# Performance work log

Measured on AMD Instinct MI355X. Metric: run time of the kernel, lower is better.

The kernel has to match this reference:

```python
import jax, jax.numpy as jnp
import numpy as np

B, S, D = 4, 1024, 1024
NH, DH = 16, 64
DI = 4096
EPS = 1e-5


def layer_norm(x, g, b):
    mu = jnp.mean(x, axis=-1, keepdims=True)
    var = jnp.mean(jnp.square(x - mu), axis=-1, keepdims=True)
    return (x - mu) * jax.lax.rsqrt(var + EPS) * g + b


def rel_shift(x):
    # x: [B, n, q, r] -> Transformer-XL relative shift + lower-tri mask
    b, n, q, r = x.shape
    zp = jnp.zeros((b, n, q, 1), x.dtype)
    xp = jnp.concatenate([zp, x], axis=3).reshape(b, n, r + 1, q)
    x = xp[:, :, 1:, :].reshape(b, n, q, r)
    tril = jnp.tril(jnp.ones((q, r), x.dtype), r - q)
    return x * tril[None, None]


def setup_inputs() -> dict:
    key = jax.random.key(0)
    ks = jax.random.split(key, 16)
    sc = 0.02
    return {
        "w": jax.random.normal(ks[0], (B, S, D), jnp.float32),
        "r": jax.random.normal(ks[1], (B, S, D), jnp.float32),
        "w_bias": jax.random.normal(ks[2], (NH, 1, DH), jnp.float32) * sc,
        "r_bias": jax.random.normal(ks[3], (NH, 1, DH), jnp.float32) * sc,
        "Wq": jax.random.normal(ks[4], (D, NH * DH), jnp.float32) * sc,
        "Wk": jax.random.normal(ks[5], (D, NH * DH), jnp.float32) * sc,
        "Wv": jax.random.normal(ks[6], (D, NH * DH), jnp.float32) * sc,
        "Wr": jax.random.normal(ks[7], (D, NH * DH), jnp.float32) * sc,
        "Wo": jax.random.normal(ks[8], (NH * DH, D), jnp.float32) * sc,
        "ln1_g": jnp.ones((D,), jnp.float32),
        "ln1_b": jnp.zeros((D,), jnp.float32),
        "W1": jax.random.normal(ks[9], (D, DI), jnp.float32) * sc,
        "b1": jnp.zeros((DI,), jnp.float32),
        "W2": jax.random.normal(ks[10], (DI, D), jnp.float32) * sc,
        "b2": jnp.zeros((D,), jnp.float32),
        "ln2_g": jnp.ones((D,), jnp.float32),
        "ln2_b": jnp.zeros((D,), jnp.float32),
    }


def reference(w, r, w_bias, r_bias, Wq, Wk, Wv, Wr, Wo,
              ln1_g, ln1_b, W1, b1, W2, b2, ln2_g, ln2_b):
    b, q_len, _ = w.shape
    k_len = q_len
    scale = 1.0 / (DH ** 0.5)

    def heads(x):
        return x.reshape(b, -1, NH, DH).transpose(0, 2, 1, 3)  # [B, n, S, d]

    q = heads(w @ Wq)
    k = heads(w @ Wk)
    v = heads(w @ Wv)
    rr = heads(r @ Wr)

    ac = jnp.einsum('bnid,bnjd->bnij', q + w_bias[None], k)
    bd = rel_shift(jnp.einsum('bnid,bnjd->bnij', q + r_bias[None], rr))
    attn_score = (ac + bd) * scale

    mask = jnp.triu(jnp.ones((q_len, k_len), bool), 1)
    attn_score = jnp.where(mask[None, None], jnp.float32(-1e9), attn_score)
    attn_prob = jax.nn.softmax(attn_score, axis=-1)

    attn_vec = jnp.einsum('bnij,bnjd->bnid', attn_prob, v)
    attn_vec = attn_vec.transpose(0, 2, 1, 3).reshape(b, q_len, NH * DH)
    attn_out = attn_vec @ Wo

    x = layer_norm(w + attn_out, ln1_g, ln1_b)
    ff = jax.nn.relu(x @ W1 + b1) @ W2 + b2
    return layer_norm(x + ff, ln2_g, ln2_b)
```

## Files before the change

### kernel.cpp

```cpp
#include <hip/hip_runtime.h>
#include <hip/hip_bf16.h>

using bf16 = __hip_bfloat16;
typedef __attribute__((ext_vector_type(8))) short bf16x8;
typedef __attribute__((ext_vector_type(4))) float f32x4;

static constexpr int TB  = 4;
static constexpr int TS  = 1024;
static constexpr int TD  = 1024;
static constexpr int TNH = 16;
static constexpr int TDH = 64;
static constexpr int TDI = 4096;

__device__ __forceinline__ void gll16(const bf16* g, bf16* l)
{
    __builtin_amdgcn_global_load_lds(
        (const __attribute__((address_space(1))) void*)g,
        (__attribute__((address_space(3))) void*)l, 16, 0, 0);
}

__global__ __launch_bounds__(256) void zero_out_k(float* __restrict__ out, long n)
{
    long i = (long)blockIdx.x * 256 + threadIdx.x;
    if (i < n) out[i] = 0.0f;
}

__global__ __launch_bounds__(256) void convert2_f2b(const float* __restrict__ a,
                                                    const float* __restrict__ b,
                                                    bf16* __restrict__ oa,
                                                    bf16* __restrict__ ob, long n)
{
    const float* src = blockIdx.y ? b : a;
    bf16* dst = blockIdx.y ? ob : oa;
    long i = ((long)blockIdx.x * 256 + threadIdx.x) * 8;
    if (i >= n) return;
    float4 f0 = *(const float4*)(src + i);
    float4 f1 = *(const float4*)(src + i + 4);
    bf16 t[8] = {__float2bfloat16(f0.x), __float2bfloat16(f0.y),
                 __float2bfloat16(f0.z), __float2bfloat16(f0.w),
                 __float2bfloat16(f1.x), __float2bfloat16(f1.y),
                 __float2bfloat16(f1.z), __float2bfloat16(f1.w)};
    *(bf16x8*)(dst + i) = *(bf16x8*)t;
}

__global__ __launch_bounds__(256) void transpose_f2b(const float* __restrict__ in,
                                                     bf16* __restrict__ out,
                                                     int R, int C)
{
    __shared__ float tile[32][33];
    int c0 = blockIdx.x * 32, r0 = blockIdx.y * 32;
    int tx = threadIdx.x & 31, ty = threadIdx.x >> 5;
#pragma unroll
    for (int dy = 0; dy < 32; dy += 8)
        tile[ty + dy][tx] = in[(long)(r0 + ty + dy) * C + (c0 + tx)];
    __syncthreads();
#pragma unroll
    for (int dy = 0; dy < 32; dy += 8)
        out[(long)(c0 + ty + dy) * R + (r0 + tx)] = __float2bfloat16(tile[tx][ty + dy]);
}

__global__ __launch_bounds__(256) void transpose5_f2b(const float* __restrict__ p0,
                                                      const float* __restrict__ p1,
                                                      const float* __restrict__ p2,
                                                      const float* __restrict__ p3,
                                                      const float* __restrict__ p4,
                                                      bf16* __restrict__ dstBase)
{
    __shared__ float tile[32][33];
    const int D = TD;
    int z = blockIdx.z;
    const float* in = (z == 0) ? p0 : (z == 1) ? p1 : (z == 2) ? p2 : (z == 3) ? p3 : p4;
    bf16* out = dstBase + (long)z * D * D;
    int c0 = blockIdx.x * 32, r0 = blockIdx.y * 32;
    int tx = threadIdx.x & 31, ty = threadIdx.x >> 5;
#pragma unroll
    for (int dy = 0; dy < 32; dy += 8)
        tile[ty + dy][tx] = in[(long)(r0 + ty + dy) * D + (c0 + tx)];
    __syncthreads();
#pragma unroll
    for (int dy = 0; dy < 32; dy += 8)
        out[(long)(c0 + ty + dy) * D + (r0 + tx)] = __float2bfloat16(tile[tx][ty + dy]);
}

__global__ __launch_bounds__(256) void transpose_v(const bf16* __restrict__ V,
                                                   bf16* __restrict__ VT)
{
    __shared__ bf16 tile[32][33];
    int bn = blockIdx.z;
    int b = bn >> 4, n = bn & 15;
    const bf16* src = V + ((long)b * TS) * (TNH * TDH) + n * TDH;
    bf16* dst = VT + (long)bn * TDH * TS;
    int s0 = blockIdx.x * 32, d0 = blockIdx.y * 32;
    int tx = threadIdx.x & 31, ty = threadIdx.x >> 5;
#pragma unroll
    for (int dy = 0; dy < 32; dy += 8)
        tile[ty + dy][tx] = src[(long)(s0 + ty + dy) * (TNH * TDH) + (d0 + tx)];
    __syncthreads();
#pragma unroll
    for (int dy = 0; dy < 32; dy += 8)
        dst[(long)(d0 + ty + dy) * TS + (s0 + tx)] = tile[tx][ty + dy];
}


__device__ __forceinline__ void stage_half(const bf16* __restrict__ X, long ldx,
                                           long rbase, long kcol,
                                           bf16* lds, int srow)
{
    gll16(X + (rbase + srow) * ldx + kcol, lds);
    gll16(X + (rbase + 128 + srow) * ldx + kcol, lds + 4096);
}

template<int MODE>
__global__ __launch_bounds__(512, 2) void gemm256_k(
    const bf16* __restrict__ A, long lda,
    const bf16* __restrict__ Bt, long ldb,
    bf16* __restrict__ O0, bf16* __restrict__ O1,
    bf16* __restrict__ O2, bf16* __restrict__ O3,
    float* __restrict__ F0, float* __restrict__ F1,
    float* __restrict__ F2, float* __restrict__ F3,
    const float* __restrict__ bias,
    int Kz, int GY, long ldc)
{
    __shared__ bf16 LDSbf[65536];

    const int z = blockIdx.y;
    const long kb = (long)z * Kz;
    const int NT = Kz >> 6;
    const int NI = NT >> 1;

    const int nwg = gridDim.x;
    const int orig = blockIdx.x;
    const int q = nwg >> 3, r = nwg & 7;
    const int xcd = orig & 7, idx = orig >> 3;
    const int wgid = (xcd < r ? xcd * (q + 1) : r * (q + 1) + (xcd - r) * q) + idx;

    int tx, ty;
    if (MODE == 1) {
        if (wgid < 192) { ty = wgid & 15; tx = wgid >> 4; }
        else { int w2 = wgid - 192; ty = 16 + (w2 & 15); tx = 12 + (w2 >> 4); }
    } else {
        ty = wgid % GY; tx = wgid / GY;
    }
    const long row0 = (long)ty * 256;
    const int col0 = tx * 256;

    const int tid = threadIdx.x;
    const int lane = tid & 63;
    const int wave = tid >> 6;
    const int wm2 = wave >> 2;
    const int wn4 = wave & 3;
    const int l15 = lane & 15;
    const int lq  = lane >> 4;

    const int slot = ((l15 & 1) << 2) | (lq ^ ((l15 >> 1) & 3));
    const int rdA = (wm2 * 64 + (l15 >> 1)) * 64 + slot * 8;
    const int rdB = 16384 + (wn4 * 32 + (l15 >> 1)) * 64 + slot * 8;

    const int srow  = wave * 16 + ((lane >> 3) << 1) + ((lane >> 2) & 1);
    const int scol8 = ((lane & 3) ^ ((lane >> 3) & 3)) * 8;

    f32x4 acc[8][4] = {};
    bf16x8 af[8], bb[4];

#define SA(t, db, kh) stage_half(A, lda, row0, kb + (long)(t) * 64 + (kh) * 32 + scol8, \
                                 LDSbf + (db) * 32768 + (kh) * 8192 + wave * 512, srow)
#define SB(t, db, kh) stage_half(Bt, ldb, (long)col0, kb + (long)(t) * 64 + (kh) * 32 + scol8, \
                                 LDSbf + (db) * 32768 + 16384 + (kh) * 8192 + wave * 512, srow)
#define RD_A(bp, kh) do {                                                              \
    _Pragma("unroll")                                                                  \
    for (int i_ = 0; i_ < 8; ++i_)                                                     \
        af[i_] = *(const bf16x8*)(LDSbf + (bp) * 32768 + (kh) * 8192 + rdA + i_ * 512);\
    } while (0)
#define RD_B(bp, kh, jh) do {                                                          \
    bb[(jh)*2]   = *(const bf16x8*)(LDSbf + (bp)*32768 + (kh)*8192 + rdB + ((jh)*2)*512);   \
    bb[(jh)*2+1] = *(const bf16x8*)(LDSbf + (bp)*32768 + (kh)*8192 + rdB + ((jh)*2+1)*512); \
    } while (0)
#define MM(jh) do {                                                                    \
    __builtin_amdgcn_s_setprio(1);                                                     \
    _Pragma("unroll")                                                                  \
    for (int i_ = 0; i_ < 8; ++i_) {                                                   \
        acc[i_][(jh)*2]   = __builtin_amdgcn_mfma_f32_16x16x32_bf16(af[i_], bb[(jh)*2],   acc[i_][(jh)*2],   0, 0, 0); \
        acc[i_][(jh)*2+1] = __builtin_amdgcn_mfma_f32_16x16x32_bf16(af[i_], bb[(jh)*2+1], acc[i_][(jh)*2+1], 0, 0, 0); \
    }                                                                                  \
    __builtin_amdgcn_s_setprio(0);                                                     \
    } while (0)
#define BAR       __builtin_amdgcn_s_barrier()
#define WLGKM0    do { asm volatile("s_waitcnt lgkmcnt(0)" ::: "memory");              \
                       __builtin_amdgcn_sched_barrier(0); } while (0)
#define WVM6      asm volatile("s_waitcnt vmcnt(6)" ::: "memory")

    SA(0, 0, 0); SB(0, 0, 0); SA(0, 0, 1); SB(0, 0, 1); SA(1, 1, 0);
    WVM6; BAR;

    for (int it = 0; it < NI; ++it) {
        const int T  = 2 * it;
        const int t1 = T + 1;
        const int t2 = (T + 2 < NT) ? T + 2 : NT - 1;
        const int t3 = (T + 3 < NT) ? T + 3 : NT - 1;

        RD_A(0, 0); RD_B(0, 0, 0); SB(t1, 1, 0);
        BAR; WLGKM0; MM(0); BAR;
        RD_B(0, 0, 1); SA(t1, 1, 1);
        BAR; WLGKM0; MM(1); WVM6; BAR;
        RD_A(0, 1); RD_B(0, 1, 0); SB(t1, 1, 1);
        BAR; WLGKM0; MM(0); BAR;
        RD_B(0, 1, 1); SA(t2, 0, 0);
        BAR; WLGKM0; MM(1); WVM6; BAR;
        RD_A(1, 0); RD_B(1, 0, 0); SB(t2, 0, 0);
        BAR; WLGKM0; MM(0); BAR;
        RD_B(1, 0, 1); SA(t2, 0, 1);
        BAR; WLGKM0; MM(1); WVM6; BAR;
        RD_A(1, 1); RD_B(1, 1, 0); SB(t2, 0, 1);
        BAR; WLGKM0; MM(0); BAR;
        RD_B(1, 1, 1); SA(t3, 1, 0);
        BAR; WLGKM0; MM(1); WVM6; BAR;
    }
    asm volatile("s_waitcnt vmcnt(0)" ::: "memory");

#undef SA
#undef SB
#undef RD_A
#undef RD_B
#undef MM
#undef BAR
#undef WLGKM0
#undef WVM6

    if (MODE == 0) {
        float* F = (z == 0) ? F0 : (z == 1) ? F1 : (z == 2) ? F2 : F3;
#pragma unroll
        for (int i = 0; i < 8; ++i) {
            long rb = (row0 + wm2 * 128 + i * 16 + lq * 4) * ldc;
#pragma unroll
            for (int j = 0; j < 4; ++j) {
                int nc = col0 + wn4 * 64 + j * 16 + l15;
#pragma unroll
                for (int rg = 0; rg < 4; ++rg)
                    F[rb + (long)rg * ldc + nc] = acc[i][j][rg];
            }
        }
    } else if (MODE == 1) {
        const int sel = tx >> 2;
        bf16* O = (sel == 0) ? O0 : (sel == 1) ? O1 : (sel == 2) ? O2 : O3;
        const int coladj = sel << 10;
        const long rowadj = (sel == 3) ? 4096 : 0;
#pragma unroll
        for (int i = 0; i < 8; ++i) {
            long rb = (row0 - rowadj + wm2 * 128 + i * 16 + lq * 4) * 1024;
#pragma unroll
            for (int j = 0; j < 4; ++j) {
                int nc = col0 - coladj + wn4 * 64 + j * 16 + l15;
#pragma unroll
                for (int rg = 0; rg < 4; ++rg) {
                    float v = acc[i][j][rg];
                    if (sel == 0) v += bias[nc];
                    O[rb + (long)rg * 1024 + nc] = __float2bfloat16(v);
                }
            }
        }
    } else {
#pragma unroll
        for (int i = 0; i < 8; ++i) {
            long rb = (row0 + wm2 * 128 + i * 16 + lq * 4) * ldc;
#pragma unroll
            for (int j = 0; j < 4; ++j) {
                int nc = col0 + wn4 * 64 + j * 16 + l15;
#pragma unroll
                for (int rg = 0; rg < 4; ++rg) {
                    float v = acc[i][j][rg] + bias[nc];
                    v = fmaxf(v, 0.0f);
                    O0[rb + (long)rg * ldc + nc] = __float2bfloat16(v);
                }
            }
        }
    }
}

__global__ __launch_bounds__(256, 1) void flash_attn(
    const bf16* __restrict__ Qw, const bf16* __restrict__ Kb,
    const bf16* __restrict__ RRb, const bf16* __restrict__ VT,
    const float* __restrict__ wbias, const float* __restrict__ rbias,
    bf16* __restrict__ Oa)
{
    const int S = TS, D = TD;
    __shared__ bf16 Ks[128 * 64];
    __shared__ bf16 RRs[256 * 64];
    __shared__ bf16 VTs[64 * 128];
    __shared__ bf16 SCR[4][32 * 161];

    const int bx = blockIdx.x;
    const int irev = bx >> 6, bn = bx & 63;
    const int it = 7 - irev;
    const int i0 = it * 128;
    const int b = bn >> 4, n = bn & 15;

    const int tid = threadIdx.x, lane = tid & 63, wave = tid >> 6;
    const int dw = wave * 32;
    const int l15 = lane & 15, lq = lane >> 4;
    const int sr8 = lane >> 3, sc8 = lane & 7;
    const int vr4 = lane >> 4, vc16 = lane & 15;

    bf16x8 afw[2][2], afr[2][2];
#pragma unroll
    for (int m = 0; m < 2; ++m)
#pragma unroll
        for (int ks = 0; ks < 2; ++ks) {
            const bf16* qp = Qw + ((long)(b * S + i0 + dw + 16 * m + l15)) * D
                             + n * 64 + ks * 32 + lq * 8;
            afw[m][ks] = *(const bf16x8*)qp;
            bf16 tmp[8];
#pragma unroll
            for (int jj = 0; jj < 8; ++jj) {
                int di_ = n * 64 + ks * 32 + lq * 8 + jj;
                float f = __bfloat162float(((const bf16*)&afw[m][ks])[jj])
                          + rbias[di_] - wbias[di_];
                tmp[jj] = __float2bfloat16(f);
            }
            afr[m][ks] = *(bf16x8*)tmp;
        }

    float mst[2][4], lst[2][4];
    f32x4 Oacc[2][4] = {};
#pragma unroll
    for (int m = 0; m < 2; ++m)
#pragma unroll
        for (int rg = 0; rg < 4; ++rg) { mst[m][rg] = -1e30f; lst[m][rg] = 0.0f; }

    bf16* scr = &SCR[wave][0];
    const int cofs = 96 - dw;

    for (int jt = 0; jt <= it; ++jt) {
        const int j0 = jt * 128;
        const int cT0 = S - 1 + j0 - i0 - 127;

#pragma unroll
        for (int c = 0; c < 4; ++c) {
            int ch = wave * 4 + c;
            int row = ch * 8 + sr8;
            int cbs = sc8 ^ (sr8 & 7);
            gll16(Kb + ((long)(b * S + j0 + row)) * D + n * 64 + cbs * 8, &Ks[ch * 512]);
        }
#pragma unroll
        for (int c = 0; c < 8; ++c) {
            int ch = wave * 8 + c;
            int row = ch * 8 + sr8;
            int grow = cT0 + row; if (grow > S - 1) grow = S - 1;
            int cbs = sc8 ^ (sr8 & 7);
            gll16(RRb + ((long)(b * S + grow)) * D + n * 64 + cbs * 8, &RRs[ch * 512]);
        }
#pragma unroll
        for (int c = 0; c < 4; ++c) {
            int ch = wave * 4 + c;
            int row = ch * 4 + vr4;
            int cbs = vc16 ^ (row & 15);
            gll16(VT + ((long)(bn * 64 + row)) * S + j0 + cbs * 8, &VTs[ch * 512]);
        }
        __syncthreads();

        f32x4 bd[2][10] = {};
#pragma unroll
        for (int ks = 0; ks < 2; ++ks) {
            bf16x8 bfr[10];
#pragma unroll
            for (int nf = 0; nf < 10; ++nf) {
                int row = cofs + nf * 16 + l15;
                int cb = ks * 4 + lq;
                bfr[nf] = *(const bf16x8*)(&RRs[row * 64 + (cb ^ (row & 7)) * 8]);
            }
#pragma unroll
            for (int m = 0; m < 2; ++m)
#pragma unroll
                for (int nf = 0; nf < 10; ++nf)
                    bd[m][nf] = __builtin_amdgcn_mfma_f32_16x16x32_bf16(
                        afr[m][ks], bfr[nf], bd[m][nf], 0, 0, 0);
        }
#pragma unroll
        for (int m = 0; m < 2; ++m)
#pragma unroll
            for (int nf = 0; nf < 10; ++nf)
#pragma unroll
                for (int rg = 0; rg < 4; ++rg) {
                    int ldi = lq * 4 + rg + 16 * m;
                    scr[ldi * 161 + nf * 16 + l15] = __float2bfloat16(bd[m][nf][rg]);
                }

        f32x4 ac[2][8] = {};
#pragma unroll
        for (int ks = 0; ks < 2; ++ks) {
            bf16x8 bk[8];
#pragma unroll
            for (int nf = 0; nf < 8; ++nf) {
                int row = nf * 16 + l15;
                int cb = ks * 4 + lq;
                bk[nf] = *(const bf16x8*)(&Ks[row * 64 + (cb ^ (row & 7)) * 8]);
            }
#pragma unroll
            for (int m = 0; m < 2; ++m)
#pragma unroll
                for (int nf = 0; nf < 8; ++nf)
                    ac[m][nf] = __builtin_amdgcn_mfma_f32_16x16x32_bf16(
                        afw[m][ks], bk[nf], ac[m][nf], 0, 0, 0);
        }

        const bool diag = (jt == it);
#pragma unroll
        for (int m = 0; m < 2; ++m)
#pragma unroll
            for (int nf = 0; nf < 8; ++nf)
#pragma unroll
                for (int rg = 0; rg < 4; ++rg) {
                    int ldi = lq * 4 + rg + 16 * m;
                    int col = nf * 16 + l15;
                    float bdv = __bfloat162float(scr[ldi * 161 + (col + 31 - ldi)]);
                    float s = (ac[m][nf][rg] + bdv) * 0.125f;
                    if (diag && (col > dw + ldi)) s = -1e30f;
                    ac[m][nf][rg] = s;
                }

        float alpha[2][4];
#pragma unroll
        for (int m = 0; m < 2; ++m)
#pragma unroll
            for (int rg = 0; rg < 4; ++rg) {
                float v = -1e30f;
#pragma unroll
                for (int nf = 0; nf < 8; ++nf) v = fmaxf(v, ac[m][nf][rg]);
                for (int o = 8; o; o >>= 1) v = fmaxf(v, __shfl_xor(v, o));
                float mn = fmaxf(mst[m][rg], v);
                alpha[m][rg] = __expf(mst[m][rg] - mn);
                mst[m][rg] = mn;
            }
#pragma unroll
        for (int m = 0; m < 2; ++m)
#pragma unroll
            for (int nf = 0; nf < 8; ++nf)
#pragma unroll
                for (int rg = 0; rg < 4; ++rg)
                    ac[m][nf][rg] = __expf(ac[m][nf][rg] - mst[m][rg]);
#pragma unroll
        for (int m = 0; m < 2; ++m)
#pragma unroll
            for (int rg = 0; rg < 4; ++rg) {
                float sv = 0.0f;
#pragma unroll
                for (int nf = 0; nf < 8; ++nf) sv += ac[m][nf][rg];
                for (int o = 8; o; o >>= 1) sv += __shfl_xor(sv, o);
                lst[m][rg] = lst[m][rg] * alpha[m][rg] + sv;
            }
#pragma unroll
        for (int m = 0; m < 2; ++m)
#pragma unroll
            for (int nf = 0; nf < 4; ++nf)
#pragma unroll
                for (int rg = 0; rg < 4; ++rg)
                    Oacc[m][nf][rg] *= alpha[m][rg];

#pragma unroll
        for (int m = 0; m < 2; ++m)
#pragma unroll
            for (int nf = 0; nf < 8; ++nf)
#pragma unroll
                for (int rg = 0; rg < 4; ++rg) {
                    int ldi = lq * 4 + rg + 16 * m;
                    scr[ldi * 136 + nf * 16 + l15] = __float2bfloat16(ac[m][nf][rg]);
                }
#pragma unroll
        for (int ks2 = 0; ks2 < 4; ++ks2) {
            bf16x8 pa[2];
#pragma unroll
            for (int m = 0; m < 2; ++m)
                pa[m] = *(const bf16x8*)(&scr[(16 * m + l15) * 136 + ks2 * 32 + lq * 8]);
            bf16x8 vb[4];
#pragma unroll
            for (int nf = 0; nf < 4; ++nf) {
                int row = nf * 16 + l15;
                int cb = ks2 * 4 + lq;
                vb[nf] = *(const bf16x8*)(&VTs[row * 128 + (cb ^ (row & 15)) * 8]);
            }
#pragma unroll
            for (int m = 0; m < 2; ++m)
#pragma unroll
                for (int nf = 0; nf < 4; ++nf)
                    Oacc[m][nf] = __builtin_amdgcn_mfma_f32_16x16x32_bf16(
                        pa[m], vb[nf], Oacc[m][nf], 0, 0, 0);
        }
        __syncthreads();
    }

#pragma unroll
    for (int m = 0; m < 2; ++m)
#pragma unroll
        for (int rg = 0; rg < 4; ++rg) {
            float inv = 1.0f / lst[m][rg];
#pragma unroll
            for (int nf = 0; nf < 4; ++nf) {
                int row = i0 + dw + lq * 4 + rg + 16 * m;
                int col = nf * 16 + l15;
                Oa[((long)(b * S + row)) * D + n * 64 + col] =
                    __float2bfloat16(Oacc[m][nf][rg] * inv);
            }
        }
}

__global__ __launch_bounds__(256) void layernorm_f(const float* __restrict__ A0,
                                                   const float* __restrict__ A1,
                                                   const float* __restrict__ A2,
                                                   const float* __restrict__ A3,
                                                   const float* __restrict__ bias,
                                                   const float* __restrict__ residf,
                                                   const bf16* __restrict__ residb,
                                                   const float* __restrict__ g,
                                                   const float* __restrict__ beta,
                                                   float* __restrict__ Yf,
                                                   bf16* __restrict__ Yb)
{
    const int D = TD;
    long row = blockIdx.x;
    int tid = threadIdx.x;
    int wave = tid >> 6;

    float v[4], s = 0.0f;
#pragma unroll
    for (int it = 0; it < 4; ++it) {
        int c = tid + it * 256;
        float x = A0[row * D + c] + A1[row * D + c] + A2[row * D + c] + A3[row * D + c];
        if (bias)   x += bias[c];
        if (residf) x += residf[row * D + c];
        if (residb) x += __bfloat162float(residb[row * D + c]);
        v[it] = x; s += x;
    }
    for (int off = 32; off; off >>= 1) s += __shfl_xor(s, off);
    __shared__ float sm[8];
    if ((tid & 63) == 0) sm[wave] = s;
    __syncthreads();
    float mean = (sm[0] + sm[1] + sm[2] + sm[3]) * (1.0f / D);

    float var = 0.0f;
#pragma unroll
    for (int it = 0; it < 4; ++it) { float d = v[it] - mean; var += d * d; }
    for (int off = 32; off; off >>= 1) var += __shfl_xor(var, off);
    if ((tid & 63) == 0) sm[4 + wave] = var;
    __syncthreads();
    var = (sm[4] + sm[5] + sm[6] + sm[7]) * (1.0f / D);
    float rinv = rsqrtf(var + 1e-5f);

#pragma unroll
    for (int it = 0; it < 4; ++it) {
        int c = tid + it * 256;
        float o = (v[it] - mean) * rinv * g[c] + beta[c];
        if (Yf) Yf[row * D + c] = o;
        if (Yb) Yb[row * D + c] = __float2bfloat16(o);
    }
}

extern "C" void kernel_launch(void* const* d_in, const int* in_sizes, int n_in,
                              void* d_out, int out_size, void* d_ws, size_t ws_size,
                              hipStream_t stream)
{
    const float* w      = (const float*)d_in[0];
    const float* r      = (const float*)d_in[1];
    const float* w_bias = (const float*)d_in[2];
    const float* r_bias = (const float*)d_in[3];
    const float* Wq     = (const float*)d_in[4];
    const float* Wk     = (const float*)d_in[5];
    const float* Wv     = (const float*)d_in[6];
    const float* Wr     = (const float*)d_in[7];
    const float* Wo     = (const float*)d_in[8];
    const float* ln1_g  = (const float*)d_in[9];
    const float* ln1_b  = (const float*)d_in[10];
    const float* W1     = (const float*)d_in[11];
    const float* b1     = (const float*)d_in[12];
    const float* W2     = (const float*)d_in[13];
    const float* b2     = (const float*)d_in[14];
    const float* ln2_g  = (const float*)d_in[15];
    const float* ln2_b  = (const float*)d_in[16];
    float* out = (float*)d_out;

    const int  B = TB, S = TS, D = TD, NH = TNH, DH = TDH, DI = TDI;
    const long MS = (long)B * S;
    const long ND = (long)MS * D;

    char* base = (char*)d_ws;
    size_t off = 0;
    auto alloc = [&](size_t bytes) -> void* {
        void* p = base + off;
        off += (bytes + 255) & ~(size_t)255;
        return p;
    };
    bf16* wqT  = (bf16*)alloc(2UL * D * D);
    bf16* wkT  = (bf16*)alloc(2UL * D * D);
    bf16* wvT  = (bf16*)alloc(2UL * D * D);
    bf16* wrT  = (bf16*)alloc(2UL * D * D);
    bf16* woT  = (bf16*)alloc(2UL * D * D);
    bf16* w1T  = (bf16*)alloc(2UL * D * DI);
    bf16* w2T  = (bf16*)alloc(2UL * DI * D);
    bf16* bufA = (bf16*)alloc(2UL * ND);
    bf16* bufB = (bf16*)alloc(2UL * ND);
    bf16* Qw   = (bf16*)alloc(2UL * ND);
    bf16* Kb   = (bf16*)alloc(2UL * ND);
    bf16* RRb  = (bf16*)alloc(2UL * ND);
    bf16* VT   = (bf16*)alloc(2UL * ND);
    bf16* R0   = (bf16*)alloc(2UL * MS * DI);
    size_t need = off;
    (void)in_sizes; (void)n_in; (void)out_size;

    if (ws_size < need) {
        zero_out_k<<<dim3((unsigned)((ND + 255) / 256)), 256, 0, stream>>>(out, ND);
        return;
    }

    bf16* w_bf = bufA;  bf16* attn_vec = bufA;
    bf16* r_bf = bufB;  bf16* x_bf     = bufB;
    bf16* Vb   = R0;    bf16* h        = R0;
    float* Pf  = (float*)Qw;

    convert2_f2b<<<dim3((unsigned)(ND / (8 * 256)), 2), 256, 0, stream>>>(
        w, r, w_bf, r_bf, ND);
    transpose5_f2b<<<dim3(D / 32, D / 32, 5), 256, 0, stream>>>(
        Wq, Wk, Wv, Wr, Wo, wqT);
    transpose_f2b<<<dim3(DI / 32, D / 32), 256, 0, stream>>>(W1, w1T, D, DI);
    transpose_f2b<<<dim3(D / 32, DI / 32), 256, 0, stream>>>(W2, w2T, DI, D);

    gemm256_k<1><<<dim3(256, 1), 512, 0, stream>>>(
        w_bf, D, wqT, D, Qw, Kb, Vb, RRb,
        nullptr, nullptr, nullptr, nullptr, w_bias, D, 16, D);
    transpose_v<<<dim3(S / 32, DH / 32, B * NH), 256, 0, stream>>>(Vb, VT);

    flash_attn<<<dim3(512), 256, 0, stream>>>(Qw, Kb, RRb, VT, w_bias, r_bias, attn_vec);

    gemm256_k<0><<<dim3(64, 4), 512, 0, stream>>>(
        attn_vec, D, woT, D, nullptr, nullptr, nullptr, nullptr,
        Pf, Pf + ND, Pf + 2 * ND, Pf + 3 * ND, nullptr, D / 4, 16, D);
    layernorm_f<<<dim3((unsigned)MS), 256, 0, stream>>>(
        Pf, Pf + ND, Pf + 2 * ND, Pf + 3 * ND, nullptr, w, nullptr,
        ln1_g, ln1_b, nullptr, x_bf);

    gemm256_k<2><<<dim3(256, 1), 512, 0, stream>>>(
        x_bf, D, w1T, D, h, nullptr, nullptr, nullptr,
        nullptr, nullptr, nullptr, nullptr, b1, D, 16, DI);

    gemm256_k<0><<<dim3(64, 4), 512, 0, stream>>>(
        h, DI, w2T, DI, nullptr, nullptr, nullptr, nullptr,
        Pf, Pf + ND, (float*)wqT, out, nullptr, DI / 4, 16, D);
    layernorm_f<<<dim3((unsigned)MS), 256, 0, stream>>>(
        Pf, Pf + ND, (float*)wqT, out, b2, nullptr, x_bf,
        ln2_g, ln2_b, out, nullptr);
}
```

Before: 410.5 us.

## Pack Q/K/R/V into MFMA fragment layout and run attention as single-wave blocks

The QKV projection epilogue and the V transpose now write Q, K, RR and V in a per-head packed layout that matches the MFMA fragment order. The flash-attention kernel becomes one wave per block (2048 blocks) and reads K, RR and V fragments straight from global memory instead of staging them through shared memory. This drops the LDS staging and the block barriers, and the block index is remapped so that heads are grouped per XCD for L2 locality. In exchange each wave issues its own uncoalesced global reads and loses LDS reuse across waves, which increases L2 traffic.

```diff
diff --git a/kernel.cpp b/kernel.cpp
--- a/kernel.cpp
+++ b/kernel.cpp
@@ -83,13 +83,13 @@
 }
 
 __global__ __launch_bounds__(256) void transpose_v(const bf16* __restrict__ V,
-                                                   bf16* __restrict__ VT)
+                                                   bf16* __restrict__ Vpk)
 {
     __shared__ bf16 tile[32][33];
     int bn = blockIdx.z;
     int b = bn >> 4, n = bn & 15;
     const bf16* src = V + ((long)b * TS) * (TNH * TDH) + n * TDH;
-    bf16* dst = VT + (long)bn * TDH * TS;
+    bf16* dst = Vpk + (long)bn * 65536;
     int s0 = blockIdx.x * 32, d0 = blockIdx.y * 32;
     int tx = threadIdx.x & 31, ty = threadIdx.x >> 5;
 #pragma unroll
@@ -97,8 +97,11 @@
         tile[ty + dy][tx] = src[(long)(s0 + ty + dy) * (TNH * TDH) + (d0 + tx)];
     __syncthreads();
 #pragma unroll
-    for (int dy = 0; dy < 32; dy += 8)
-        dst[(long)(d0 + ty + dy) * TS + (s0 + tx)] = tile[tx][ty + dy];
+    for (int dy = 0; dy < 32; dy += 8) {
+        int d = d0 + ty + dy, s = s0 + tx;
+        dst[((d >> 4) * 128 + (s >> 3)) * 128 + (d & 15) * 8 + (s & 7)] =
+            tile[tx][ty + dy];
+    }
 }
 
 
@@ -246,7 +249,7 @@
         const long rowadj = (sel == 3) ? 4096 : 0;
 #pragma unroll
         for (int i = 0; i < 8; ++i) {
-            long rb = (row0 - rowadj + wm2 * 128 + i * 16 + lq * 4) * 1024;
+            long mrow0 = row0 - rowadj + wm2 * 128 + i * 16 + lq * 4;
 #pragma unroll
             for (int j = 0; j < 4; ++j) {
                 int nc = col0 - coladj + wn4 * 64 + j * 16 + l15;
@@ -254,7 +257,18 @@
                 for (int rg = 0; rg < 4; ++rg) {
                     float v = acc[i][j][rg];
                     if (sel == 0) v += bias[nc];
-                    O[rb + (long)rg * 1024 + nc] = __float2bfloat16(v);
+                    long mrow = mrow0 + rg;
+                    if (sel == 2) {
+                        O[mrow * 1024 + nc] = __float2bfloat16(v);
+                    } else {
+                        long b_ = mrow >> 10;
+                        int s  = (int)mrow & 1023;
+                        int n_ = nc >> 6, d = nc & 63;
+                        long pidx = ((b_ * 16 + n_) << 16)
+                                  + ((s >> 4) * 8 + (d >> 3)) * 128
+                                  + (s & 15) * 8 + (d & 7);
+                        O[pidx] = __float2bfloat16(v);
+                    }
                 }
             }
         }
@@ -276,38 +290,39 @@
     }
 }
 
-__global__ __launch_bounds__(256, 1) void flash_attn(
-    const bf16* __restrict__ Qw, const bf16* __restrict__ Kb,
-    const bf16* __restrict__ RRb, const bf16* __restrict__ VT,
+__global__ __launch_bounds__(64, 2) void flash_attn(
+    const bf16* __restrict__ Qpk, const bf16* __restrict__ Kpk,
+    const bf16* __restrict__ RRpk, const bf16* __restrict__ Vpk,
     const float* __restrict__ wbias, const float* __restrict__ rbias,
     bf16* __restrict__ Oa)
 {
     const int S = TS, D = TD;
-    __shared__ bf16 Ks[128 * 64];
-    __shared__ bf16 RRs[256 * 64];
-    __shared__ bf16 VTs[64 * 128];
-    __shared__ bf16 SCR[4][32 * 161];
-
-    const int bx = blockIdx.x;
-    const int irev = bx >> 6, bn = bx & 63;
-    const int it = 7 - irev;
+    __shared__ bf16 scr[32 * 161];
+
+    const int orig = blockIdx.x;
+    const int xcd = orig & 7, idx = orig >> 3;
+    const int bn = xcd * 8 + (idx & 7);
+    const int rem = idx >> 3;
+    const int it = 7 - (rem >> 2);
+    const int dw = (rem & 3) * 32;
     const int i0 = it * 128;
     const int b = bn >> 4, n = bn & 15;
 
-    const int tid = threadIdx.x, lane = tid & 63, wave = tid >> 6;
-    const int dw = wave * 32;
+    const int lane = threadIdx.x;
     const int l15 = lane & 15, lq = lane >> 4;
-    const int sr8 = lane >> 3, sc8 = lane & 7;
-    const int vr4 = lane >> 4, vc16 = lane & 15;
+
+    const bf16* Qb = Qpk  + (long)bn * 65536;
+    const bf16* Kb = Kpk  + (long)bn * 65536;
+    const bf16* Rb = RRpk + (long)bn * 65536;
+    const bf16* Vb = Vpk  + (long)bn * 65536;
 
     bf16x8 afw[2][2], afr[2][2];
 #pragma unroll
     for (int m = 0; m < 2; ++m)
 #pragma unroll
         for (int ks = 0; ks < 2; ++ks) {
-            const bf16* qp = Qw + ((long)(b * S + i0 + dw + 16 * m + l15)) * D
-                             + n * 64 + ks * 32 + lq * 8;
-            afw[m][ks] = *(const bf16x8*)qp;
+            afw[m][ks] = *(const bf16x8*)(
+                Qb + ((((i0 + dw) >> 4) + m) * 8 + ks * 4 + lq) * 128 + l15 * 8);
             bf16 tmp[8];
 #pragma unroll
             for (int jj = 0; jj < 8; ++jj) {
@@ -326,80 +341,57 @@
 #pragma unroll
         for (int rg = 0; rg < 4; ++rg) { mst[m][rg] = -1e30f; lst[m][rg] = 0.0f; }
 
-    bf16* scr = &SCR[wave][0];
-    const int cofs = 96 - dw;
+    const int cofsg = 992 - i0 - dw;
 
     for (int jt = 0; jt <= it; ++jt) {
         const int j0 = jt * 128;
-        const int cT0 = S - 1 + j0 - i0 - 127;
-
-#pragma unroll
-        for (int c = 0; c < 4; ++c) {
-            int ch = wave * 4 + c;
-            int row = ch * 8 + sr8;
-            int cbs = sc8 ^ (sr8 & 7);
-            gll16(Kb + ((long)(b * S + j0 + row)) * D + n * 64 + cbs * 8, &Ks[ch * 512]);
-        }
-#pragma unroll
-        for (int c = 0; c < 8; ++c) {
-            int ch = wave * 8 + c;
-            int row = ch * 8 + sr8;
-            int grow = cT0 + row; if (grow > S - 1) grow = S - 1;
-            int cbs = sc8 ^ (sr8 & 7);
-            gll16(RRb + ((long)(b * S + grow)) * D + n * 64 + cbs * 8, &RRs[ch * 512]);
-        }
-#pragma unroll
-        for (int c = 0; c < 4; ++c) {
-            int ch = wave * 4 + c;
-            int row = ch * 4 + vr4;
-            int cbs = vc16 ^ (row & 15);
-            gll16(VT + ((long)(bn * 64 + row)) * S + j0 + cbs * 8, &VTs[ch * 512]);
-        }
-        __syncthreads();
-
-        f32x4 bd[2][10] = {};
-#pragma unroll
-        for (int ks = 0; ks < 2; ++ks) {
-            bf16x8 bfr[10];
-#pragma unroll
-            for (int nf = 0; nf < 10; ++nf) {
-                int row = cofs + nf * 16 + l15;
-                int cb = ks * 4 + lq;
-                bfr[nf] = *(const bf16x8*)(&RRs[row * 64 + (cb ^ (row & 7)) * 8]);
+        const int rbt = (j0 + cofsg) >> 4;
+
+#pragma unroll
+        for (int g = 0; g < 2; ++g) {
+            f32x4 bdl[2][5] = {};
+#pragma unroll
+            for (int ks = 0; ks < 2; ++ks) {
+                bf16x8 bfr[5];
+#pragma unroll
+                for (int f = 0; f < 5; ++f) {
+                    int t = rbt + g * 5 + f;
+                    if (t > 63) t = 63;
+                    bfr[f] = *(const bf16x8*)(Rb + (t * 8 + ks * 4 + lq) * 128 + l15 * 8);
+                }
+#pragma unroll
+                for (int m = 0; m < 2; ++m)
+#pragma unroll
+                    for (int f = 0; f < 5; ++f)
+                        bdl[m][f] = __builtin_amdgcn_mfma_f32_16x16x32_bf16(
+                            afr[m][ks], bfr[f], bdl[m][f], 0, 0, 0);
             }
 #pragma unroll
             for (int m = 0; m < 2; ++m)
 #pragma unroll
-                for (int nf = 0; nf < 10; ++nf)
-                    bd[m][nf] = __builtin_amdgcn_mfma_f32_16x16x32_bf16(
-                        afr[m][ks], bfr[nf], bd[m][nf], 0, 0, 0);
-        }
-#pragma unroll
-        for (int m = 0; m < 2; ++m)
-#pragma unroll
-            for (int nf = 0; nf < 10; ++nf)
-#pragma unroll
-                for (int rg = 0; rg < 4; ++rg) {
-                    int ldi = lq * 4 + rg + 16 * m;
-                    scr[ldi * 161 + nf * 16 + l15] = __float2bfloat16(bd[m][nf][rg]);
-                }
+                for (int f = 0; f < 5; ++f)
+#pragma unroll
+                    for (int rg = 0; rg < 4; ++rg) {
+                        int ldi = lq * 4 + rg + 16 * m;
+                        scr[ldi * 161 + (g * 5 + f) * 16 + l15] =
+                            __float2bfloat16(bdl[m][f][rg]);
+                    }
+        }
 
         f32x4 ac[2][8] = {};
 #pragma unroll
         for (int ks = 0; ks < 2; ++ks) {
             bf16x8 bk[8];
 #pragma unroll
-            for (int nf = 0; nf < 8; ++nf) {
-                int row = nf * 16 + l15;
-                int cb = ks * 4 + lq;
-                bk[nf] = *(const bf16x8*)(&Ks[row * 64 + (cb ^ (row & 7)) * 8]);
-            }
+            for (int f = 0; f < 8; ++f)
+                bk[f] = *(const bf16x8*)(
+                    Kb + (((j0 >> 4) + f) * 8 + ks * 4 + lq) * 128 + l15 * 8);
 #pragma unroll
             for (int m = 0; m < 2; ++m)
 #pragma unroll
-                for (int nf = 0; nf < 8; ++nf)
-                    ac[m][nf] = __builtin_amdgcn_mfma_f32_16x16x32_bf16(
-                        afw[m][ks], bk[nf], ac[m][nf], 0, 0, 0);
+                for (int f = 0; f < 8; ++f)
+                    ac[m][f] = __builtin_amdgcn_mfma_f32_16x16x32_bf16(
+                        afw[m][ks], bk[f], ac[m][f], 0, 0, 0);
         }
 
         const bool diag = (jt == it);
@@ -472,11 +464,9 @@
                 pa[m] = *(const bf16x8*)(&scr[(16 * m + l15) * 136 + ks2 * 32 + lq * 8]);
             bf16x8 vb[4];
 #pragma unroll
-            for (int nf = 0; nf < 4; ++nf) {
-                int row = nf * 16 + l15;
-                int cb = ks2 * 4 + lq;
-                vb[nf] = *(const bf16x8*)(&VTs[row * 128 + (cb ^ (row & 15)) * 8]);
-            }
+            for (int nf = 0; nf < 4; ++nf)
+                vb[nf] = *(const bf16x8*)(
+                    Vb + (nf * 128 + (j0 >> 3) + ks2 * 4 + lq) * 128 + l15 * 8);
 #pragma unroll
             for (int m = 0; m < 2; ++m)
 #pragma unroll
@@ -484,7 +474,6 @@
                     Oacc[m][nf] = __builtin_amdgcn_mfma_f32_16x16x32_bf16(
                         pa[m], vb[nf], Oacc[m][nf], 0, 0, 0);
         }
-        __syncthreads();
     }
 
 #pragma unroll
@@ -596,10 +585,10 @@
     bf16* w2T  = (bf16*)alloc(2UL * DI * D);
     bf16* bufA = (bf16*)alloc(2UL * ND);
     bf16* bufB = (bf16*)alloc(2UL * ND);
-    bf16* Qw   = (bf16*)alloc(2UL * ND);
-    bf16* Kb   = (bf16*)alloc(2UL * ND);
-    bf16* RRb  = (bf16*)alloc(2UL * ND);
-    bf16* VT   = (bf16*)alloc(2UL * ND);
+    bf16* Qpk  = (bf16*)alloc(2UL * ND);
+    bf16* Kpk  = (bf16*)alloc(2UL * ND);
+    bf16* RRpk = (bf16*)alloc(2UL * ND);
+    bf16* Vpk  = (bf16*)alloc(2UL * ND);
     bf16* R0   = (bf16*)alloc(2UL * MS * DI);
     size_t need = off;
     (void)in_sizes; (void)n_in; (void)out_size;
@@ -612,7 +601,7 @@
     bf16* w_bf = bufA;  bf16* attn_vec = bufA;
     bf16* r_bf = bufB;  bf16* x_bf     = bufB;
     bf16* Vb   = R0;    bf16* h        = R0;
-    float* Pf  = (float*)Qw;
+    float* Pf  = (float*)Qpk;
 
     convert2_f2b<<<dim3((unsigned)(ND / (8 * 256)), 2), 256, 0, stream>>>(
         w, r, w_bf, r_bf, ND);
@@ -622,11 +611,12 @@
     transpose_f2b<<<dim3(D / 32, DI / 32), 256, 0, stream>>>(W2, w2T, DI, D);
 
     gemm256_k<1><<<dim3(256, 1), 512, 0, stream>>>(
-        w_bf, D, wqT, D, Qw, Kb, Vb, RRb,
+        w_bf, D, wqT, D, Qpk, Kpk, Vb, RRpk,
         nullptr, nullptr, nullptr, nullptr, w_bias, D, 16, D);
-    transpose_v<<<dim3(S / 32, DH / 32, B * NH), 256, 0, stream>>>(Vb, VT);
-
-    flash_attn<<<dim3(512), 256, 0, stream>>>(Qw, Kb, RRb, VT, w_bias, r_bias, attn_vec);
+    transpose_v<<<dim3(S / 32, DH / 32, B * NH), 256, 0, stream>>>(Vb, Vpk);
+
+    flash_attn<<<dim3(2048), 64, 0, stream>>>(Qpk, Kpk, RRpk, Vpk, w_bias, r_bias,
+                                              attn_vec);
 
     gemm256_k<0><<<dim3(64, 4), 512, 0, stream>>>(
         attn_vec, D, woT, D, nullptr, nullptr, nullptr, nullptr,
```

After: 411.1 us. About the same (+0.1%).
